# Kernel tuning notes

Measured on AMD Instinct MI355X. Metric: run time of the kernel, lower is better.

The kernel has to match this reference:

```python
import jax, jax.numpy as jnp
import numpy as np

N = 50000          # nodes (cells)
G = 1000           # input genes
E = 800000         # edges
HIDDEN = 128
HEADS = 8
C_HID = HIDDEN // HEADS   # 16 per-head channels
LATENT = 16
NEG_SLOPE = 0.2


def _gat_layer(x, src, dst, W, a_src, a_dst, b, heads, out_ch, concat):
    """PyG GATConv (shared lin for src/dst, add_self_loops=False, eval mode)."""
    n = x.shape[0]
    h = (x @ W).reshape(n, heads, out_ch)                 # [N,H,C]
    al_s = jnp.einsum('nhc,hc->nh', h, a_src)             # [N,H]
    al_d = jnp.einsum('nhc,hc->nh', h, a_dst)             # [N,H]
    logits = jax.nn.leaky_relu(al_s[src] + al_d[dst], NEG_SLOPE)  # [E,H]
    # segment softmax over destination neighborhoods
    m = jax.ops.segment_max(logits, dst, num_segments=n)  # [N,H]
    m = jnp.where(jnp.isfinite(m), m, 0.0)                # empty segments -> 0
    e = jnp.exp(logits - m[dst])                          # [E,H]
    denom = jax.ops.segment_sum(e, dst, num_segments=n)   # [N,H]
    alpha = e / (denom[dst] + 1e-16)                      # [E,H]
    msg = h[src] * alpha[:, :, None]                      # [E,H,C]
    out = jax.ops.segment_sum(msg, dst, num_segments=n)   # [N,H,C]
    out = out.reshape(n, heads * out_ch) if concat else out.mean(axis=1)
    return out + b


def setup_inputs() -> dict:
    key = jax.random.key(0)
    ks = jax.random.split(key, 16)
    x = jax.random.normal(ks[0], (N, G), dtype=jnp.float32)
    edge_index = jax.random.randint(ks[1], (2, E), 0, N, dtype=jnp.int64)

    def glorot(k, shape):
        fan_in, fan_out = shape[0], shape[-1]
        s = jnp.sqrt(6.0 / (fan_in + fan_out)).astype(jnp.float32)
        return jax.random.uniform(k, shape, jnp.float32, -s, s)

    # layer 0: G -> 8 heads x 16 (concat -> 128)
    W0 = glorot(ks[2], (G, HEADS * C_HID))
    as0 = glorot(ks[3], (HEADS, C_HID))
    ad0 = glorot(ks[4], (HEADS, C_HID))
    b0 = jnp.zeros((HEADS * C_HID,), jnp.float32)
    # layer 1: 128 -> 8 heads x 16 (concat -> 128)
    W1 = glorot(ks[5], (HIDDEN, HEADS * C_HID))
    as1 = glorot(ks[6], (HEADS, C_HID))
    ad1 = glorot(ks[7], (HEADS, C_HID))
    b1 = jnp.zeros((HEADS * C_HID,), jnp.float32)
    # layer 2: 128 -> 1 head x 16 (concat=False -> 16)
    W2 = glorot(ks[8], (HIDDEN, LATENT))
    as2 = glorot(ks[9], (1, LATENT))
    ad2 = glorot(ks[10], (1, LATENT))
    b2 = jnp.zeros((LATENT,), jnp.float32)

    return {"x": x, "edge_index": edge_index,
            "W0": W0, "as0": as0, "ad0": ad0, "b0": b0,
            "W1": W1, "as1": as1, "ad1": ad1, "b1": b1,
            "W2": W2, "as2": as2, "ad2": ad2, "b2": b2}


def reference(x, edge_index, W0, as0, ad0, b0, W1, as1, ad1, b1, W2, as2, ad2, b2):
    src, dst = edge_index[0], edge_index[1]
    h = _gat_layer(x, src, dst, W0, as0, ad0, b0, HEADS, C_HID, concat=True)
    h = jax.nn.elu(h)
    h = _gat_layer(h, src, dst, W1, as1, ad1, b1, HEADS, C_HID, concat=True)
    h = jax.nn.elu(h)
    z = _gat_layer(h, src, dst, W2, as2, ad2, b2, 1, LATENT, concat=False)
    return z
```

## Files before the change

### kernel.cpp

```cpp
#include <hip/hip_runtime.h>
#include <hip/hip_bf16.h>
#include <math.h>

#define GENES 1000

typedef __attribute__((ext_vector_type(8))) _Float16 half8;
typedef __attribute__((ext_vector_type(4))) float f32x4;
typedef __attribute__((ext_vector_type(4))) unsigned int uint4v;
typedef __attribute__((ext_vector_type(2))) unsigned int uint2v;

__device__ inline float f16lo(unsigned int v) {
  return (float)__builtin_bit_cast(_Float16, (unsigned short)(v & 0xffffu));
}
__device__ inline float f16hi(unsigned int v) {
  return (float)__builtin_bit_cast(_Float16, (unsigned short)(v >> 16));
}
__device__ inline unsigned int pk(float a, float b) {
  return __builtin_bit_cast(unsigned int, __builtin_amdgcn_cvt_pkrtz(a, b));
}

__device__ inline void gload16(const void* g, void* l) {
  __builtin_amdgcn_global_load_lds(
      (const __attribute__((address_space(1))) unsigned int*)g,
      (__attribute__((address_space(3))) unsigned int*)l, 16, 0, 0);
}


__global__ void k_deg(const int* __restrict__ ei, int* __restrict__ deg, int E) {
  int e = blockIdx.x * blockDim.x + threadIdx.x;
  if (e < E) atomicAdd(&deg[ei[E + e]], 1);
}

__global__ void k_scan1(int* __restrict__ deg, int* __restrict__ ptr,
                        int* __restrict__ bsum, int n) {
  __shared__ int ws[4];
  int t = threadIdx.x, b = blockIdx.x;
  int i = b * 256 + t;
  int lane = t & 63, w = t >> 6;
  int x = 0;
  if (i < n) { x = deg[i]; deg[i] = 0; }
  #pragma unroll
  for (int d = 1; d < 64; d <<= 1) {
    int y = __shfl_up(x, d);
    if (lane >= d) x += y;
  }
  if (lane == 63) ws[w] = x;
  __syncthreads();
  if (t == 0) {
    int s = 0;
    #pragma unroll
    for (int k = 0; k < 4; ++k) { s += ws[k]; ws[k] = s; }
  }
  __syncthreads();
  int incl = x + (w ? ws[w - 1] : 0);
  if (i < n) ptr[i + 1] = incl;
  if (t == 255) bsum[b] = incl;
  if (i == 0) ptr[0] = 0;
}

__global__ void k_scan2(int* __restrict__ bsum, int nb) {
  __shared__ int ws[4];
  int t = threadIdx.x;
  int lane = t & 63, w = t >> 6;
  int v = (t < nb) ? bsum[t] : 0;
  int x = v;
  #pragma unroll
  for (int d = 1; d < 64; d <<= 1) {
    int y = __shfl_up(x, d);
    if (lane >= d) x += y;
  }
  if (lane == 63) ws[w] = x;
  __syncthreads();
  if (t == 0) {
    int s = 0;
    #pragma unroll
    for (int k = 0; k < 4; ++k) { s += ws[k]; ws[k] = s; }
  }
  __syncthreads();
  int incl = x + (w ? ws[w - 1] : 0);
  if (t < nb) bsum[t] = incl - v;
}

__global__ void k_scan3(int* __restrict__ ptr, const int* __restrict__ bsum, int n) {
  int i = blockIdx.x * 256 + threadIdx.x;
  if (i < n) ptr[i + 1] += bsum[blockIdx.x];
}

__global__ void k_scatter(const int* __restrict__ ei, const int* __restrict__ ptr,
                          int* __restrict__ cur, int* __restrict__ srcs, int E) {
  int e = blockIdx.x * blockDim.x + threadIdx.x;
  if (e >= E) return;
  int d = ei[E + e];
  int pos = ptr[d] + atomicAdd(&cur[d], 1);
  srcs[pos] = ei[e];
}


__global__ void k_wpackall(const float* __restrict__ W0, const float* __restrict__ W1,
                           const float* __restrict__ W2, unsigned short* __restrict__ P,
                           int K0) {
  int t = blockIdx.x * blockDim.x + threadIdx.x;
  if (t >= 163840) return;
  const float* W; int K, N, e;
  if (t < 131072)      { W = W0; K = K0;  N = 128; e = t; }
  else if (t < 147456) { W = W1; K = 128; N = 128; e = t - 131072; }
  else                 { W = W2; K = 128; N = 16;  e = t - 147456; }
  int s = e >> 12, rem = e & 4095;
  int q = rem >> 10, col = (rem >> 3) & 127, j = rem & 7;
  int k = s * 32 + q * 8 + j;
  float v = (k < K && col < N) ? W[(long)k * N + col] : 0.f;
  _Float16 h = (_Float16)v;
  P[t] = __builtin_bit_cast(unsigned short, h);
}


__global__ __launch_bounds__(512) void k_mgemm11(
    const float* __restrict__ A, const unsigned short* __restrict__ Pb,
    unsigned short* __restrict__ outp, float* __restrict__ als,
    float* __restrict__ ald, const float* __restrict__ avs,
    const float* __restrict__ avd, int M, int K) {
  __shared__ __align__(16) char lds[32768];

  int t = threadIdx.x, lane = t & 63, wv = t >> 6;
  int r15 = lane & 15, q = lane >> 4;
  int wr = wv >> 1, wc = wv & 1;
  long row0 = (long)blockIdx.x * 64;

  int srow = wv * 8 + (lane >> 3);
  int sseg = lane & 7;
  int gseg = sseg ^ (srow & 7);
  long arow = row0 + srow; if (arow >= M) arow = M - 1;
  const char* gA = (const char*)(A + arow * (long)K) + gseg * 16;
  const char* gB = (const char*)Pb + t * 16;

  f32x4 acc[4];
  #pragma unroll
  for (int nt = 0; nt < 4; ++nt) acc[nt] = (f32x4){0.f, 0.f, 0.f, 0.f};

  auto issue = [&](int s) {
    char* Ab = lds + (s & 1) * 8192;
    char* Bb = lds + 16384 + (s & 1) * 8192;
    gload16(gA + (size_t)s * 128, Ab + t * 16);
    gload16(gB + (size_t)s * 8192, Bb + t * 16);
  };
  auto compute = [&](int s) {
    const char* Ab = lds + (s & 1) * 8192;
    const char* Bb = lds + 16384 + (s & 1) * 8192;
    int row = wr * 16 + r15;
    int sw = row & 7;
    uint4v alo = *(const uint4v*)(Ab + row * 128 + ((2 * q) ^ sw) * 16);
    uint4v ahi = *(const uint4v*)(Ab + row * 128 + ((2 * q + 1) ^ sw) * 16);
    float4 lo = __builtin_bit_cast(float4, alo);
    float4 hi = __builtin_bit_cast(float4, ahi);
    uint4v au;
    au[0] = pk(lo.x, lo.y); au[1] = pk(lo.z, lo.w);
    au[2] = pk(hi.x, hi.y); au[3] = pk(hi.z, hi.w);
    half8 af = __builtin_bit_cast(half8, au);
    #pragma unroll
    for (int nt = 0; nt < 4; ++nt) {
      half8 bf = *(const half8*)(Bb + q * 2048 + (wc * 64 + nt * 16 + r15) * 16);
      acc[nt] = __builtin_amdgcn_mfma_f32_16x16x32_f16(af, bf, acc[nt], 0, 0, 0);
    }
  };

  issue(0);
  __syncthreads();
  for (int s = 0; s < 32; ++s) {
    if (s + 1 < 32) issue(s + 1);
    compute(s);
    __syncthreads();
  }

  long rbase = row0 + wr * 16 + q * 4;
  #pragma unroll
  for (int i = 0; i < 4; ++i) {
    long r = rbase + i;
    if (r < M) {
      #pragma unroll
      for (int nt = 0; nt < 4; ++nt) {
        int col = wc * 64 + nt * 16 + r15;
        _Float16 hv = (_Float16)acc[nt][i];
        outp[r * 128 + col] = __builtin_bit_cast(unsigned short, hv);
      }
    }
  }
  #pragma unroll
  for (int nt = 0; nt < 4; ++nt) {
    int head = wc * 4 + nt;
    float cs = avs[head * 16 + r15];
    float cd = avd[head * 16 + r15];
    #pragma unroll
    for (int i = 0; i < 4; ++i) {
      float s1 = acc[nt][i] * cs;
      float s2 = acc[nt][i] * cd;
      #pragma unroll
      for (int d = 1; d < 16; d <<= 1) {
        s1 += __shfl_xor(s1, d);
        s2 += __shfl_xor(s2, d);
      }
      if (r15 == 0) {
        long r = rbase + i;
        if (r < M) { als[r * 8 + head] = s1; ald[r * 8 + head] = s2; }
      }
    }
  }
}


template<int HH, bool AF16, bool OF16>
__global__ __launch_bounds__(512) void k_mgemm7(
    const void* __restrict__ Ap, const unsigned short* __restrict__ Pb,
    void* __restrict__ outp, float* __restrict__ als, float* __restrict__ ald,
    const float* __restrict__ avs, const float* __restrict__ avd,
    int M, int K, int nst, int ldc) {
  __shared__ __align__(16) char lds[24576];
  char* bA0 = lds;
  char* bA1 = lds + 4096;
  char* bB0 = lds + 8192;
  char* bB1 = lds + 16384;

  int t = threadIdx.x, lane = t & 63;
  int r15 = lane & 15, q = lane >> 4;
  int wv = t >> 6;
  int wr = wv >> 1, wc = wv & 1;
  long row0 = (long)blockIdx.x * 64;

  int srow = t >> 3, sseg = t & 7;
  long arow = row0 + srow; if (arow >= M) arow = M - 1;
  const float* pa32 = (const float*)Ap + arow * (long)K;
  const unsigned short* pa16 = (const unsigned short*)Ap + arow * (long)K;

  f32x4 acc[4];
  #pragma unroll
  for (int nt = 0; nt < 4; ++nt) acc[nt] = (f32x4){0.f, 0.f, 0.f, 0.f};

  uint4v rA0, rA1, rB0, rB1;
  uint2v sA0, sA1;

  auto loadA = [&](int s, uint4v& r32, uint2v& r16) {
    int k0 = s * 32 + sseg * 4;
    if constexpr (AF16) {
      r16 = (k0 < K) ? *(const uint2v*)(pa16 + k0) : (uint2v){0u, 0u};
    } else {
      r32 = (k0 < K) ? *(const uint4v*)(pa32 + k0) : (uint4v){0u, 0u, 0u, 0u};
    }
  };
  auto writeA = [&](char* buf, uint4v r32, uint2v r16) {
    char* p = buf + ((sseg >> 1) * 1024 + srow * 16 + (sseg & 1) * 8);
    if constexpr (AF16) {
      *(uint2v*)p = r16;
    } else {
      float4 f = __builtin_bit_cast(float4, r32);
      uint2v h;
      h[0] = pk(f.x, f.y);
      h[1] = pk(f.z, f.w);
      *(uint2v*)p = h;
    }
  };
  auto loadB = [&](int s, uint4v& r) {
    r = *(const uint4v*)(Pb + (size_t)s * 4096 + t * 8);
  };
  auto writeB = [&](char* buf, uint4v r) {
    *(uint4v*)(buf + t * 16) = r;
  };
  auto compute = [&](const char* bA, const char* bB) {
    half8 af = *(const half8*)(bA + q * 1024 + (wr * 16 + r15) * 16);
    #pragma unroll
    for (int nt = 0; nt < 4; ++nt) {
      half8 bf = *(const half8*)(bB + q * 2048 + (wc * 64 + nt * 16 + r15) * 16);
      acc[nt] = __builtin_amdgcn_mfma_f32_16x16x32_f16(af, bf, acc[nt], 0, 0, 0);
    }
  };

  loadA(0, rA0, sA0); loadB(0, rB0);
  if (nst > 1) { loadA(1, rA1, sA1); loadB(1, rB1); }
  writeA(bA0, rA0, sA0); writeB(bB0, rB0);
  __syncthreads();

  for (int s = 0; s < nst; s += 2) {
    if (s + 2 < nst) { loadA(s + 2, rA0, sA0); loadB(s + 2, rB0); }
    compute(bA0, bB0);
    if (s + 1 < nst) { writeA(bA1, rA1, sA1); writeB(bB1, rB1); }
    __syncthreads();
    if (s + 1 < nst) {
      if (s + 3 < nst) { loadA(s + 3, rA1, sA1); loadB(s + 3, rB1); }
      compute(bA1, bB1);
      if (s + 2 < nst) { writeA(bA0, rA0, sA0); writeB(bB0, rB0); }
      __syncthreads();
    }
  }

  long rbase = row0 + wr * 16 + q * 4;
  if constexpr (OF16) {
    unsigned short* o16 = (unsigned short*)outp;
    #pragma unroll
    for (int i = 0; i < 4; ++i) {
      long r = rbase + i;
      if (r < M) {
        #pragma unroll
        for (int nt = 0; nt < 4; ++nt) {
          int col = wc * 64 + nt * 16 + r15;
          _Float16 hv = (_Float16)acc[nt][i];
          o16[r * ldc + col] = __builtin_bit_cast(unsigned short, hv);
        }
      }
    }
  } else {
    float* o32 = (float*)outp;
    #pragma unroll
    for (int i = 0; i < 4; ++i) {
      long r = rbase + i;
      if (r < M) {
        #pragma unroll
        for (int nt = 0; nt < 4; ++nt) {
          int col = wc * 64 + nt * 16 + r15;
          if (col < ldc) o32[r * ldc + col] = acc[nt][i];
        }
      }
    }
  }
  #pragma unroll
  for (int nt = 0; nt < 4; ++nt) {
    int head = wc * 4 + nt;
    if (head < HH) {
      float cs = avs[head * 16 + r15];
      float cd = avd[head * 16 + r15];
      #pragma unroll
      for (int i = 0; i < 4; ++i) {
        float s1 = acc[nt][i] * cs;
        float s2 = acc[nt][i] * cd;
        #pragma unroll
        for (int d = 1; d < 16; d <<= 1) {
          s1 += __shfl_xor(s1, d);
          s2 += __shfl_xor(s2, d);
        }
        if (r15 == 0) {
          long r = rbase + i;
          if (r < M) { als[r * HH + head] = s1; ald[r * HH + head] = s2; }
        }
      }
    }
  }
}


__global__ void k_agg128h(const unsigned short* __restrict__ h,
                          const float* __restrict__ als, const float* __restrict__ ald,
                          const int* __restrict__ ptr, const int* __restrict__ srcs,
                          const float* __restrict__ bias,
                          unsigned short* __restrict__ out, int n) {
  int wid = (int)(((long)blockIdx.x * blockDim.x + threadIdx.x) >> 6);
  if (wid >= n) return;
  int lane = threadIdx.x & 63;
  int half = lane >> 5, l5 = lane & 31;
  int c0 = 4 * l5;
  int hB = l5 >> 2;
  int p0 = ptr[wid], deg = ptr[wid + 1] - p0;
  float aldB = ald[wid * 8 + hB];
  float a0 = 0.f, a1 = 0.f, a2 = 0.f, a3 = 0.f, dsum = 0.f;
  int j = half;
  for (; j + 6 < deg; j += 8) {
    int s0 = srcs[p0 + j],     s1 = srcs[p0 + j + 2];
    int s2 = srcs[p0 + j + 4], s3 = srcs[p0 + j + 6];
    float l0 = als[s0 * 8 + hB] + aldB;
    float l1 = als[s1 * 8 + hB] + aldB;
    float l2 = als[s2 * 8 + hB] + aldB;
    float l3 = als[s3 * 8 + hB] + aldB;
    uint2v h0 = *(const uint2v*)(h + (long)s0 * 128 + c0);
    uint2v h1 = *(const uint2v*)(h + (long)s1 * 128 + c0);
    uint2v h2 = *(const uint2v*)(h + (long)s2 * 128 + c0);
    uint2v h3 = *(const uint2v*)(h + (long)s3 * 128 + c0);
    l0 = l0 > 0.f ? l0 : 0.2f * l0;
    l1 = l1 > 0.f ? l1 : 0.2f * l1;
    l2 = l2 > 0.f ? l2 : 0.2f * l2;
    l3 = l3 > 0.f ? l3 : 0.2f * l3;
    float e0 = __expf(l0), e1 = __expf(l1), e2 = __expf(l2), e3 = __expf(l3);
    dsum += e0 + e1 + e2 + e3;
    a0 += e0 * f16lo(h0[0]) + e1 * f16lo(h1[0]) + e2 * f16lo(h2[0]) + e3 * f16lo(h3[0]);
    a1 += e0 * f16hi(h0[0]) + e1 * f16hi(h1[0]) + e2 * f16hi(h2[0]) + e3 * f16hi(h3[0]);
    a2 += e0 * f16lo(h0[1]) + e1 * f16lo(h1[1]) + e2 * f16lo(h2[1]) + e3 * f16lo(h3[1]);
    a3 += e0 * f16hi(h0[1]) + e1 * f16hi(h1[1]) + e2 * f16hi(h2[1]) + e3 * f16hi(h3[1]);
  }
  for (; j < deg; j += 2) {
    int s = srcs[p0 + j];
    float l = als[s * 8 + hB] + aldB;
    l = l > 0.f ? l : 0.2f * l;
    float e = __expf(l);
    uint2v hv = *(const uint2v*)(h + (long)s * 128 + c0);
    dsum += e;
    a0 += e * f16lo(hv[0]);
    a1 += e * f16hi(hv[0]);
    a2 += e * f16lo(hv[1]);
    a3 += e * f16hi(hv[1]);
  }
  a0 += __shfl_xor(a0, 32);
  a1 += __shfl_xor(a1, 32);
  a2 += __shfl_xor(a2, 32);
  a3 += __shfl_xor(a3, 32);
  dsum += __shfl_xor(dsum, 32);
  if (half == 0) {
    float inv = 1.f / (dsum + 1e-16f);
    float o0 = a0 * inv + bias[c0];
    float o1 = a1 * inv + bias[c0 + 1];
    float o2 = a2 * inv + bias[c0 + 2];
    float o3 = a3 * inv + bias[c0 + 3];
    o0 = o0 > 0.f ? o0 : (__expf(o0) - 1.f);
    o1 = o1 > 0.f ? o1 : (__expf(o1) - 1.f);
    o2 = o2 > 0.f ? o2 : (__expf(o2) - 1.f);
    o3 = o3 > 0.f ? o3 : (__expf(o3) - 1.f);
    uint2v po;
    po[0] = __builtin_bit_cast(unsigned int, __builtin_amdgcn_cvt_pkrtz(o0, o1));
    po[1] = __builtin_bit_cast(unsigned int, __builtin_amdgcn_cvt_pkrtz(o2, o3));
    *(uint2v*)(out + (long)wid * 128 + c0) = po;
  }
}


__global__ void k_agg16(const float* __restrict__ h, const float* __restrict__ als,
                        const float* __restrict__ ald, const int* __restrict__ ptr,
                        const int* __restrict__ srcs, const float* __restrict__ bias,
                        float* __restrict__ out, int n, int lda) {
  int wid = (int)(((long)blockIdx.x * blockDim.x + threadIdx.x) >> 6);
  if (wid >= n) return;
  int lane = threadIdx.x & 63;
  int p0 = ptr[wid], deg = ptr[wid + 1] - p0;
  float aldv = ald[wid];
  int g = lane >> 4, c = lane & 15;
  float acc = 0.f, dsum = 0.f;
  int j = g;
  for (; j + 12 < deg; j += 16) {
    int s0 = srcs[p0 + j],     s1 = srcs[p0 + j + 4];
    int s2 = srcs[p0 + j + 8], s3 = srcs[p0 + j + 12];
    float l0 = als[s0] + aldv, l1 = als[s1] + aldv;
    float l2 = als[s2] + aldv, l3 = als[s3] + aldv;
    float h0 = h[(long)s0 * lda + c], h1 = h[(long)s1 * lda + c];
    float h2 = h[(long)s2 * lda + c], h3 = h[(long)s3 * lda + c];
    l0 = l0 > 0.f ? l0 : 0.2f * l0;
    l1 = l1 > 0.f ? l1 : 0.2f * l1;
    l2 = l2 > 0.f ? l2 : 0.2f * l2;
    l3 = l3 > 0.f ? l3 : 0.2f * l3;
    float e0 = __expf(l0), e1 = __expf(l1), e2 = __expf(l2), e3 = __expf(l3);
    dsum += e0 + e1 + e2 + e3;
    acc += e0 * h0 + e1 * h1 + e2 * h2 + e3 * h3;
  }
  for (; j < deg; j += 4) {
    int s = srcs[p0 + j];
    float l = als[s] + aldv;
    l = l > 0.f ? l : 0.2f * l;
    float e = __expf(l);
    dsum += e;
    acc += e * h[(long)s * lda + c];
  }
  #pragma unroll
  for (int d = 16; d < 64; d <<= 1) {
    acc += __shfl_xor(acc, d);
    dsum += __shfl_xor(dsum, d);
  }
  if (lane < 16)
    out[(long)wid * 16 + lane] = acc / (dsum + 1e-16f) + bias[lane];
}


extern "C" void kernel_launch(void* const* d_in, const int* in_sizes, int n_in,
                              void* d_out, int out_size, void* d_ws, size_t ws_size,
                              hipStream_t stream) {
  const float* x  = (const float*)d_in[0];
  const int*   ei = (const int*)d_in[1];
  const float* W0 = (const float*)d_in[2];
  const float* as0= (const float*)d_in[3];
  const float* ad0= (const float*)d_in[4];
  const float* b0 = (const float*)d_in[5];
  const float* W1 = (const float*)d_in[6];
  const float* as1= (const float*)d_in[7];
  const float* ad1= (const float*)d_in[8];
  const float* b1 = (const float*)d_in[9];
  const float* W2 = (const float*)d_in[10];
  const float* as2= (const float*)d_in[11];
  const float* ad2= (const float*)d_in[12];
  const float* b2 = (const float*)d_in[13];
  float* out = (float*)d_out;

  int E = in_sizes[1] / 2;
  int n = in_sizes[0] / GENES;

  char* ws = (char*)d_ws;
  size_t off = 0;
  auto alloc = [&](size_t bytes) {
    void* p = ws + off;
    off = (off + bytes + 255) & ~(size_t)255;
    return p;
  };
  int* ptr   = (int*)alloc((size_t)(n + 1) * sizeof(int));
  int* cur   = (int*)alloc((size_t)n * sizeof(int));
  int* bsum  = (int*)alloc(512 * sizeof(int));
  int* srcs  = (int*)alloc((size_t)E * sizeof(int));
  unsigned short* Ah = (unsigned short*)alloc((size_t)n * 128 * sizeof(unsigned short));
  unsigned short* Bh = (unsigned short*)alloc((size_t)n * 128 * sizeof(unsigned short));
  float* A2  = (float*)alloc((size_t)n * 16 * sizeof(float));
  float* als = (float*)alloc((size_t)n * 8 * sizeof(float));
  float* ald = (float*)alloc((size_t)n * 8 * sizeof(float));
  unsigned short* P = (unsigned short*)alloc((size_t)163840 * sizeof(unsigned short));
  unsigned short* P0 = P;
  unsigned short* P1 = P + 131072;
  unsigned short* P2 = P + 147456;

  int eb = (E + 255) / 256;
  int nb = (n + 255) / 256;
  hipMemsetAsync(cur, 0, (size_t)n * sizeof(int), stream);
  k_deg<<<eb, 256, 0, stream>>>(ei, cur, E);
  k_scan1<<<nb, 256, 0, stream>>>(cur, ptr, bsum, n);
  k_scan2<<<1, 256, 0, stream>>>(bsum, nb);
  k_scan3<<<nb, 256, 0, stream>>>(ptr, bsum, n);
  k_scatter<<<eb, 256, 0, stream>>>(ei, ptr, cur, srcs, E);
  k_wpackall<<<640, 256, 0, stream>>>(W0, W1, W2, P, GENES);

  int mgb  = (n + 63) / 64;
  int aggb = (int)(((long)n * 64 + 255) / 256);

  k_mgemm11<<<mgb, 512, 0, stream>>>(x, P0, Ah, als, ald, as0, ad0, n, GENES);
  k_agg128h<<<aggb, 256, 0, stream>>>(Ah, als, ald, ptr, srcs, b0, Bh, n);

  k_mgemm7<8, true, true><<<mgb, 512, 0, stream>>>(
      Bh, P1, Ah, als, ald, as1, ad1, n, 128, 4, 128);
  k_agg128h<<<aggb, 256, 0, stream>>>(Ah, als, ald, ptr, srcs, b1, Bh, n);

  k_mgemm7<1, true, false><<<mgb, 512, 0, stream>>>(
      Bh, P2, A2, als, ald, as2, ad2, n, 128, 4, 16);
  k_agg16<<<aggb, 256, 0, stream>>>(A2, als, ald, ptr, srcs, b2, out, n, 16);
}
```

Before: 273.4 us.

## Fuse CSR build steps into weight-pack and first GEMM, retile layer-0 GEMM

The degree-count atomics now run inside the weight-packing kernel, and the edge scatter into CSR runs at the start of the first-layer GEMM, which removes two separate launches. The layer-0 GEMM is restructured to 32-row tiles. Each block converts a full 32x1000 strip of x to f16 in LDS once, with zero padding for the K tail. B fragments are streamed from global memory into registers two steps ahead, which drops the per-step barrier and double-buffered LDS staging. In exchange, LDS use grows to about 67 KB per block, which may reduce occupancy, and the scatter atomics now compete with the GEMM's loads of x.

```diff
diff --git a/kernel.cpp b/kernel.cpp
--- a/kernel.cpp
+++ b/kernel.cpp
@@ -19,17 +19,6 @@
   return __builtin_bit_cast(unsigned int, __builtin_amdgcn_cvt_pkrtz(a, b));
 }
 
-__device__ inline void gload16(const void* g, void* l) {
-  __builtin_amdgcn_global_load_lds(
-      (const __attribute__((address_space(1))) unsigned int*)g,
-      (__attribute__((address_space(3))) unsigned int*)l, 16, 0, 0);
-}
-
-
-__global__ void k_deg(const int* __restrict__ ei, int* __restrict__ deg, int E) {
-  int e = blockIdx.x * blockDim.x + threadIdx.x;
-  if (e < E) atomicAdd(&deg[ei[E + e]], 1);
-}
 
 __global__ void k_scan1(int* __restrict__ deg, int* __restrict__ ptr,
                         int* __restrict__ bsum, int n) {
@@ -86,113 +75,123 @@
   if (i < n) ptr[i + 1] += bsum[blockIdx.x];
 }
 
-__global__ void k_scatter(const int* __restrict__ ei, const int* __restrict__ ptr,
-                          int* __restrict__ cur, int* __restrict__ srcs, int E) {
-  int e = blockIdx.x * blockDim.x + threadIdx.x;
-  if (e >= E) return;
-  int d = ei[E + e];
-  int pos = ptr[d] + atomicAdd(&cur[d], 1);
-  srcs[pos] = ei[e];
-}
-
-
-__global__ void k_wpackall(const float* __restrict__ W0, const float* __restrict__ W1,
+
+__global__ void k_wpackdeg(const float* __restrict__ W0, const float* __restrict__ W1,
                            const float* __restrict__ W2, unsigned short* __restrict__ P,
-                           int K0) {
+                           int K0, const int* __restrict__ ei, int* __restrict__ deg,
+                           int E) {
   int t = blockIdx.x * blockDim.x + threadIdx.x;
-  if (t >= 163840) return;
-  const float* W; int K, N, e;
-  if (t < 131072)      { W = W0; K = K0;  N = 128; e = t; }
-  else if (t < 147456) { W = W1; K = 128; N = 128; e = t - 131072; }
-  else                 { W = W2; K = 128; N = 16;  e = t - 147456; }
-  int s = e >> 12, rem = e & 4095;
-  int q = rem >> 10, col = (rem >> 3) & 127, j = rem & 7;
-  int k = s * 32 + q * 8 + j;
-  float v = (k < K && col < N) ? W[(long)k * N + col] : 0.f;
-  _Float16 h = (_Float16)v;
-  P[t] = __builtin_bit_cast(unsigned short, h);
-}
-
-
-__global__ __launch_bounds__(512) void k_mgemm11(
+  if (t < 163840) {
+    const float* W; int K, N, e;
+    if (t < 131072)      { W = W0; K = K0;  N = 128; e = t; }
+    else if (t < 147456) { W = W1; K = 128; N = 128; e = t - 131072; }
+    else                 { W = W2; K = 128; N = 16;  e = t - 147456; }
+    int s = e >> 12, rem = e & 4095;
+    int q = rem >> 10, col = (rem >> 3) & 127, j = rem & 7;
+    int k = s * 32 + q * 8 + j;
+    float v = (k < K && col < N) ? W[(long)k * N + col] : 0.f;
+    _Float16 h = (_Float16)v;
+    P[t] = __builtin_bit_cast(unsigned short, h);
+  }
+  if (t < E) atomicAdd(&deg[ei[E + t]], 1);
+}
+
+
+__global__ __launch_bounds__(512) void k_mgemm12(
     const float* __restrict__ A, const unsigned short* __restrict__ Pb,
     unsigned short* __restrict__ outp, float* __restrict__ als,
     float* __restrict__ ald, const float* __restrict__ avs,
-    const float* __restrict__ avd, int M, int K) {
-  __shared__ __align__(16) char lds[32768];
+    const float* __restrict__ avd, int M, int K,
+    const int* __restrict__ ei, const int* __restrict__ ptr,
+    int* __restrict__ cur, int* __restrict__ srcs, int E) {
+  __shared__ __align__(16) char As[4 * 16896];
 
   int t = threadIdx.x, lane = t & 63, wv = t >> 6;
   int r15 = lane & 15, q = lane >> 4;
-  int wr = wv >> 1, wc = wv & 1;
-  long row0 = (long)blockIdx.x * 64;
-
-  int srow = wv * 8 + (lane >> 3);
-  int sseg = lane & 7;
-  int gseg = sseg ^ (srow & 7);
-  long arow = row0 + srow; if (arow >= M) arow = M - 1;
-  const char* gA = (const char*)(A + arow * (long)K) + gseg * 16;
-  const char* gB = (const char*)Pb + t * 16;
-
-  f32x4 acc[4];
-  #pragma unroll
-  for (int nt = 0; nt < 4; ++nt) acc[nt] = (f32x4){0.f, 0.f, 0.f, 0.f};
-
-  auto issue = [&](int s) {
-    char* Ab = lds + (s & 1) * 8192;
-    char* Bb = lds + 16384 + (s & 1) * 8192;
-    gload16(gA + (size_t)s * 128, Ab + t * 16);
-    gload16(gB + (size_t)s * 8192, Bb + t * 16);
-  };
-  auto compute = [&](int s) {
-    const char* Ab = lds + (s & 1) * 8192;
-    const char* Bb = lds + 16384 + (s & 1) * 8192;
-    int row = wr * 16 + r15;
-    int sw = row & 7;
-    uint4v alo = *(const uint4v*)(Ab + row * 128 + ((2 * q) ^ sw) * 16);
-    uint4v ahi = *(const uint4v*)(Ab + row * 128 + ((2 * q + 1) ^ sw) * 16);
-    float4 lo = __builtin_bit_cast(float4, alo);
-    float4 hi = __builtin_bit_cast(float4, ahi);
-    uint4v au;
-    au[0] = pk(lo.x, lo.y); au[1] = pk(lo.z, lo.w);
-    au[2] = pk(hi.x, hi.y); au[3] = pk(hi.z, hi.w);
-    half8 af = __builtin_bit_cast(half8, au);
-    #pragma unroll
-    for (int nt = 0; nt < 4; ++nt) {
-      half8 bf = *(const half8*)(Bb + q * 2048 + (wc * 64 + nt * 16 + r15) * 16);
-      acc[nt] = __builtin_amdgcn_mfma_f32_16x16x32_f16(af, bf, acc[nt], 0, 0, 0);
-    }
-  };
-
-  issue(0);
+  int rg = wv >> 2, cg = wv & 3;
+  long row0 = (long)blockIdx.x * 32;
+
+  {
+    int e = blockIdx.x * 512 + t;
+    if (e < E) {
+      int d = ei[E + e];
+      int pos = ptr[d] + atomicAdd(&cur[d], 1);
+      srcs[pos] = ei[e];
+    }
+  }
+
+  if (t < 96) {
+    int zq = 1 + (t >> 5), zr = t & 31;
+    *(uint4v*)(As + zq * 16896 + 31 * 528 + zr * 16) = (uint4v){0u, 0u, 0u, 0u};
+  }
+
+  #pragma unroll
+  for (int i = 0; i < 4; ++i) {
+    int R = wv * 4 + i;
+    long arow = row0 + R; if (arow >= M) arow = M - 1;
+    const float* base = A + arow * (long)K;
+    #pragma unroll
+    for (int inst = 0; inst < 4; ++inst) {
+      int off = inst * 256 + lane * 4;
+      if (off + 4 <= K) {
+        float4 v = *(const float4*)(base + off);
+        uint2v h;
+        h[0] = pk(v.x, v.y);
+        h[1] = pk(v.z, v.w);
+        int ks = off >> 5, qq = (off >> 3) & 3, j0 = off & 7;
+        *(uint2v*)(As + qq * 16896 + ks * 528 + R * 16 + j0 * 2) = h;
+      }
+    }
+  }
   __syncthreads();
+
+  f32x4 acc0 = (f32x4){0.f, 0.f, 0.f, 0.f};
+  f32x4 acc1 = (f32x4){0.f, 0.f, 0.f, 0.f};
+
+  const char* pBl = (const char*)Pb + q * 2048 + (cg * 32 + r15) * 16;
+  const char* pAf = As + q * 16896 + (rg * 16 + r15) * 16;
+  uint4v b00, b01, b10, b11;
+
+  auto issueB = [&](int s, int slot) {
+    const char* p = pBl + (size_t)s * 8192;
+    if (slot == 0) { b00 = *(const uint4v*)p; b01 = *(const uint4v*)(p + 256); }
+    else           { b10 = *(const uint4v*)p; b11 = *(const uint4v*)(p + 256); }
+  };
+
+  issueB(0, 0);
+  issueB(1, 1);
+  #pragma unroll
   for (int s = 0; s < 32; ++s) {
-    if (s + 1 < 32) issue(s + 1);
-    compute(s);
-    __syncthreads();
-  }
-
-  long rbase = row0 + wr * 16 + q * 4;
+    half8 af = *(const half8*)(pAf + s * 528);
+    uint4v bn0 = (s & 1) ? b10 : b00;
+    uint4v bn1 = (s & 1) ? b11 : b01;
+    if (s + 2 < 32) issueB(s + 2, s & 1);
+    acc0 = __builtin_amdgcn_mfma_f32_16x16x32_f16(af, __builtin_bit_cast(half8, bn0), acc0, 0, 0, 0);
+    acc1 = __builtin_amdgcn_mfma_f32_16x16x32_f16(af, __builtin_bit_cast(half8, bn1), acc1, 0, 0, 0);
+  }
+
+  long rbase = row0 + rg * 16 + q * 4;
   #pragma unroll
   for (int i = 0; i < 4; ++i) {
     long r = rbase + i;
     if (r < M) {
-      #pragma unroll
-      for (int nt = 0; nt < 4; ++nt) {
-        int col = wc * 64 + nt * 16 + r15;
-        _Float16 hv = (_Float16)acc[nt][i];
-        outp[r * 128 + col] = __builtin_bit_cast(unsigned short, hv);
-      }
-    }
-  }
-  #pragma unroll
-  for (int nt = 0; nt < 4; ++nt) {
-    int head = wc * 4 + nt;
+      int col0 = cg * 32 + r15;
+      _Float16 h0 = (_Float16)acc0[i];
+      _Float16 h1 = (_Float16)acc1[i];
+      outp[r * 128 + col0]      = __builtin_bit_cast(unsigned short, h0);
+      outp[r * 128 + col0 + 16] = __builtin_bit_cast(unsigned short, h1);
+    }
+  }
+  #pragma unroll
+  for (int nt = 0; nt < 2; ++nt) {
+    int head = cg * 2 + nt;
     float cs = avs[head * 16 + r15];
     float cd = avd[head * 16 + r15];
     #pragma unroll
     for (int i = 0; i < 4; ++i) {
-      float s1 = acc[nt][i] * cs;
-      float s2 = acc[nt][i] * cd;
+      float av = nt ? acc1[i] : acc0[i];
+      float s1 = av * cs;
+      float s2 = av * cd;
       #pragma unroll
       for (int d = 1; d < 16; d <<= 1) {
         s1 += __shfl_xor(s1, d);
@@ -507,17 +506,17 @@
   int eb = (E + 255) / 256;
   int nb = (n + 255) / 256;
   hipMemsetAsync(cur, 0, (size_t)n * sizeof(int), stream);
-  k_deg<<<eb, 256, 0, stream>>>(ei, cur, E);
+  k_wpackdeg<<<eb, 256, 0, stream>>>(W0, W1, W2, P, GENES, ei, cur, E);
   k_scan1<<<nb, 256, 0, stream>>>(cur, ptr, bsum, n);
   k_scan2<<<1, 256, 0, stream>>>(bsum, nb);
   k_scan3<<<nb, 256, 0, stream>>>(ptr, bsum, n);
-  k_scatter<<<eb, 256, 0, stream>>>(ei, ptr, cur, srcs, E);
-  k_wpackall<<<640, 256, 0, stream>>>(W0, W1, W2, P, GENES);
-
+
+  int mgb0 = (n + 31) / 32;
   int mgb  = (n + 63) / 64;
   int aggb = (int)(((long)n * 64 + 255) / 256);
 
-  k_mgemm11<<<mgb, 512, 0, stream>>>(x, P0, Ah, als, ald, as0, ad0, n, GENES);
+  k_mgemm12<<<mgb0, 512, 0, stream>>>(x, P0, Ah, als, ald, as0, ad0, n, GENES,
+                                      ei, ptr, cur, srcs, E);
   k_agg128h<<<aggb, 256, 0, stream>>>(Ah, als, ald, ptr, srcs, b0, Bh, n);
 
   k_mgemm7<8, true, true><<<mgb, 512, 0, stream>>>(
```

New measurement: 272.9 us. No clear change (-0.2%).

## Deepen first-layer GEMM pipeline to four LDS stages and fuse weight pack with degree count

Applied to the files above, without the earlier changes.

The layer-0 GEMM moves from double buffering to a 4-stage LDS ring with three tiles in flight. It replaces the two __syncthreads per step with explicit vmcnt waits plus one barrier, so global loads overlap more MFMA work. LDS per block doubles to 64KB, which may reduce occupancy. The weight-pack kernel is also merged with the degree-count kernel, saving one launch.

```diff
diff --git a/kernel.cpp b/kernel.cpp
--- a/kernel.cpp
+++ b/kernel.cpp
@@ -25,11 +25,14 @@
       (__attribute__((address_space(3))) unsigned int*)l, 16, 0, 0);
 }
 
-
-__global__ void k_deg(const int* __restrict__ ei, int* __restrict__ deg, int E) {
-  int e = blockIdx.x * blockDim.x + threadIdx.x;
-  if (e < E) atomicAdd(&deg[ei[E + e]], 1);
-}
+__device__ __forceinline__ void waitvm(int n) {
+  __builtin_amdgcn_sched_barrier(0);
+  if (n <= 0)      asm volatile("s_waitcnt vmcnt(0)" ::: "memory");
+  else if (n <= 2) asm volatile("s_waitcnt vmcnt(2)" ::: "memory");
+  else             asm volatile("s_waitcnt vmcnt(4)" ::: "memory");
+  __builtin_amdgcn_sched_barrier(0);
+}
+
 
 __global__ void k_scan1(int* __restrict__ deg, int* __restrict__ ptr,
                         int* __restrict__ bsum, int n) {
@@ -96,38 +99,40 @@
 }
 
 
-__global__ void k_wpackall(const float* __restrict__ W0, const float* __restrict__ W1,
+__global__ void k_wpackdeg(const float* __restrict__ W0, const float* __restrict__ W1,
                            const float* __restrict__ W2, unsigned short* __restrict__ P,
-                           int K0) {
+                           int K0, const int* __restrict__ ei, int* __restrict__ deg,
+                           int E) {
   int t = blockIdx.x * blockDim.x + threadIdx.x;
-  if (t >= 163840) return;
-  const float* W; int K, N, e;
-  if (t < 131072)      { W = W0; K = K0;  N = 128; e = t; }
-  else if (t < 147456) { W = W1; K = 128; N = 128; e = t - 131072; }
-  else                 { W = W2; K = 128; N = 16;  e = t - 147456; }
-  int s = e >> 12, rem = e & 4095;
-  int q = rem >> 10, col = (rem >> 3) & 127, j = rem & 7;
-  int k = s * 32 + q * 8 + j;
-  float v = (k < K && col < N) ? W[(long)k * N + col] : 0.f;
-  _Float16 h = (_Float16)v;
-  P[t] = __builtin_bit_cast(unsigned short, h);
-}
-
-
-__global__ __launch_bounds__(512) void k_mgemm11(
+  if (t < 163840) {
+    const float* W; int K, N, e;
+    if (t < 131072)      { W = W0; K = K0;  N = 128; e = t; }
+    else if (t < 147456) { W = W1; K = 128; N = 128; e = t - 131072; }
+    else                 { W = W2; K = 128; N = 16;  e = t - 147456; }
+    int s = e >> 12, rem = e & 4095;
+    int q = rem >> 10, col = (rem >> 3) & 127, j = rem & 7;
+    int k = s * 32 + q * 8 + j;
+    float v = (k < K && col < N) ? W[(long)k * N + col] : 0.f;
+    _Float16 h = (_Float16)v;
+    P[t] = __builtin_bit_cast(unsigned short, h);
+  }
+  if (t < E) atomicAdd(&deg[ei[E + t]], 1);
+}
+
+
+__global__ __launch_bounds__(512) void k_mgemm13(
     const float* __restrict__ A, const unsigned short* __restrict__ Pb,
     unsigned short* __restrict__ outp, float* __restrict__ als,
     float* __restrict__ ald, const float* __restrict__ avs,
     const float* __restrict__ avd, int M, int K) {
-  __shared__ __align__(16) char lds[32768];
+  __shared__ __align__(16) char lds[65536];
 
   int t = threadIdx.x, lane = t & 63, wv = t >> 6;
   int r15 = lane & 15, q = lane >> 4;
   int wr = wv >> 1, wc = wv & 1;
   long row0 = (long)blockIdx.x * 64;
 
-  int srow = wv * 8 + (lane >> 3);
-  int sseg = lane & 7;
+  int srow = t >> 3, sseg = t & 7;
   int gseg = sseg ^ (srow & 7);
   long arow = row0 + srow; if (arow >= M) arow = M - 1;
   const char* gA = (const char*)(A + arow * (long)K) + gseg * 16;
@@ -138,14 +143,14 @@
   for (int nt = 0; nt < 4; ++nt) acc[nt] = (f32x4){0.f, 0.f, 0.f, 0.f};
 
   auto issue = [&](int s) {
-    char* Ab = lds + (s & 1) * 8192;
-    char* Bb = lds + 16384 + (s & 1) * 8192;
+    char* Ab = lds + (s & 3) * 8192;
+    char* Bb = lds + 32768 + (s & 3) * 8192;
     gload16(gA + (size_t)s * 128, Ab + t * 16);
     gload16(gB + (size_t)s * 8192, Bb + t * 16);
   };
   auto compute = [&](int s) {
-    const char* Ab = lds + (s & 1) * 8192;
-    const char* Bb = lds + 16384 + (s & 1) * 8192;
+    const char* Ab = lds + (s & 3) * 8192;
+    const char* Bb = lds + 32768 + (s & 3) * 8192;
     int row = wr * 16 + r15;
     int sw = row & 7;
     uint4v alo = *(const uint4v*)(Ab + row * 128 + ((2 * q) ^ sw) * 16);
@@ -163,12 +168,14 @@
     }
   };
 
-  issue(0);
-  __syncthreads();
+  issue(0); issue(1); issue(2);
+  #pragma unroll
   for (int s = 0; s < 32; ++s) {
-    if (s + 1 < 32) issue(s + 1);
+    int nleft = 31 - s;
+    waitvm(nleft >= 2 ? 4 : 2 * nleft);
+    __builtin_amdgcn_s_barrier();
     compute(s);
-    __syncthreads();
+    if (s + 3 < 32) issue(s + 3);
   }
 
   long rbase = row0 + wr * 16 + q * 4;
@@ -507,17 +514,16 @@
   int eb = (E + 255) / 256;
   int nb = (n + 255) / 256;
   hipMemsetAsync(cur, 0, (size_t)n * sizeof(int), stream);
-  k_deg<<<eb, 256, 0, stream>>>(ei, cur, E);
+  k_wpackdeg<<<eb, 256, 0, stream>>>(W0, W1, W2, P, GENES, ei, cur, E);
   k_scan1<<<nb, 256, 0, stream>>>(cur, ptr, bsum, n);
   k_scan2<<<1, 256, 0, stream>>>(bsum, nb);
   k_scan3<<<nb, 256, 0, stream>>>(ptr, bsum, n);
   k_scatter<<<eb, 256, 0, stream>>>(ei, ptr, cur, srcs, E);
-  k_wpackall<<<640, 256, 0, stream>>>(W0, W1, W2, P, GENES);
 
   int mgb  = (n + 63) / 64;
   int aggb = (int)(((long)n * 64 + 255) / 256);
 
-  k_mgemm11<<<mgb, 512, 0, stream>>>(x, P0, Ah, als, ald, as0, ad0, n, GENES);
+  k_mgemm13<<<mgb, 512, 0, stream>>>(x, P0, Ah, als, ald, as0, ad0, n, GENES);
   k_agg128h<<<aggb, 256, 0, stream>>>(Ah, als, ald, ptr, srcs, b0, Bh, n);
 
   k_mgemm7<8, true, true><<<mgb, 512, 0, stream>>>(
```

New measurement: 271.8 us. No clear change (-0.6%).
